# Performance work log

Measured on AMD Instinct MI355X. Metric: run time of the kernel, lower is better.

## Reference

```python
import jax, jax.numpy as jnp
import numpy as np


def _hard_sigmoid(x):
    # Keras ConvLSTM2D default recurrent_activation
    return jnp.clip(0.2 * x + 0.5, 0.0, 1.0)


def _conv(x, w):
    # NHWC input, HWIO kernel, SAME padding, stride 1
    return jax.lax.conv_general_dilated(
        x, w, (1, 1), 'SAME', dimension_numbers=('NHWC', 'HWIO', 'NHWC'))


def _convlstm(seq, h, c, k, rk, b):
    # seq: [B, T, H, W, Cin]; h, c: [B, H, W, F]
    # k: [kh, kw, Cin, 4F], rk: [kh, kw, F, 4F], b: [4F]
    def step(carry, x):
        h, c = carry
        z = _conv(x, k) + _conv(h, rk) + b  # [B,H,W,4F]
        zi, zf, zc, zo = jnp.split(z, 4, axis=-1)
        i = _hard_sigmoid(zi)
        f = _hard_sigmoid(zf)
        o = _hard_sigmoid(zo)
        c = f * c + i * jnp.tanh(zc)
        h = o * jnp.tanh(c)
        return (h, c), None
    (h, c), _ = jax.lax.scan(step, (h, c), jnp.swapaxes(seq, 0, 1))
    return h, c


def setup_inputs() -> dict:
    key = jax.random.key(0)
    ks = jax.random.split(key, 14)
    B, T, H, W, Cin, F, K = 32, 1, 64, 64, 1, 64, 3
    s = 0.05
    inp = {
        'input_': jax.random.normal(ks[0], (B, T, H, W, Cin), jnp.float32),
        'h0': jax.random.normal(ks[1], (B, H, W, F), jnp.float32) * s,
        'c0': jax.random.normal(ks[2], (B, H, W, F), jnp.float32) * s,
        'h1': jax.random.normal(ks[3], (B, H, W, F), jnp.float32) * s,
        'c1': jax.random.normal(ks[4], (B, H, W, F), jnp.float32) * s,
        'k0': jax.random.normal(ks[5], (K, K, Cin, 4 * F), jnp.float32) * s,
        'rk0': jax.random.normal(ks[6], (K, K, F, 4 * F), jnp.float32) * s,
        'b0': jnp.zeros((4 * F,), jnp.float32),
        'k1': jax.random.normal(ks[7], (K, K, F, 4 * F), jnp.float32) * s,
        'rk1': jax.random.normal(ks[8], (K, K, F, 4 * F), jnp.float32) * s,
        'b1': jnp.zeros((4 * F,), jnp.float32),
        'cw': jax.random.normal(ks[9], (1, 1, F, 1), jnp.float32) * s,
        'cb': jnp.zeros((1,), jnp.float32),
    }
    return inp


def reference(input_, h0, c0, h1, c1, k0, rk0, b0, k1, rk1, b1, cw, cb):
    # Layer 0 consumes the input frame sequence (T=1)
    h0n, c0n = _convlstm(input_, h0, c0, k0, rk0, b0)
    # Layer 1 consumes layer-0's last hidden state as its (length-1) input
    h1n, c1n = _convlstm(h0n[:, None], h1, c1, k1, rk1, b1)
    frames = _conv(h1n, cw) + cb  # 1x1 conv head -> [B,H,W,1]
    return frames, h0n, c0n, h1n, c1n
```

## Files before the change

### kernel.cpp

```cpp
#include <hip/hip_runtime.h>
#include <hip/hip_bf16.h>

typedef short s16;
typedef __attribute__((ext_vector_type(8))) short bf16x8;
typedef __attribute__((ext_vector_type(4))) float f32x4;

__device__ __forceinline__ s16 f2bf(float f) {
  unsigned u = __builtin_bit_cast(unsigned, f);
  unsigned r = (u + 0x7FFFu + ((u >> 16) & 1u)) >> 16;
  return (s16)r;
}

__device__ __forceinline__ float hsig(float x) {
  return fminf(fmaxf(0.2f * x + 0.5f, 0.0f), 1.0f);
}

__global__ void wprep_kernel(const float* __restrict__ rk0, const float* __restrict__ k1,
                             const float* __restrict__ rk1, const float* __restrict__ k0,
                             s16* __restrict__ w0q, s16* __restrict__ w1q,
                             s16* __restrict__ w2q, s16* __restrict__ k0t) {
  int idx = blockIdx.x * 256 + threadIdx.x;
  const int n1 = 18 * 8192;
  if (idx < 3 * n1) {
    int which = idx / n1;
    int i = idx - which * n1;
    int e    = i & 7;
    int lane = (i >> 3) & 63;
    int g    = (i >> 9) & 3;
    int j    = (i >> 11) & 3;
    int k    = (i >> 13) & 1;
    int tap  = i >> 14;
    int l15 = lane & 15, l4 = lane >> 4;
    int ic = k * 32 + l4 * 8 + e;
    int oc = j * 64 + g * 16 + l15;
    const float* src = (which == 0) ? rk0 : (which == 1) ? k1 : rk1;
    s16* dst = (which == 0) ? w0q : (which == 1) ? w1q : w2q;
    dst[i] = f2bf(src[(tap * 64 + ic) * 256 + oc]);
  } else if (idx < 3 * n1 + 8192) {
    int r = idx - 3 * n1;
    int kk = r & 31;
    int oc = r >> 5;
    k0t[r] = (kk < 9) ? f2bf(k0[kk * 256 + oc]) : (s16)0;
  }
}

#define PXS 66
#define ROWSZ (PXS * 64)
#define ASZ (6 * ROWSZ)

template <bool F32>
__device__ __forceinline__ bf16x8 load_conv8(const void* src, long off) {
  if constexpr (F32) {
    const float* p = (const float*)src + off;
    float4 v0 = *reinterpret_cast<const float4*>(p);
    float4 v1 = *reinterpret_cast<const float4*>(p + 4);
    bf16x8 r;
    r[0] = f2bf(v0.x); r[1] = f2bf(v0.y); r[2] = f2bf(v0.z); r[3] = f2bf(v0.w);
    r[4] = f2bf(v1.x); r[5] = f2bf(v1.y); r[6] = f2bf(v1.z); r[7] = f2bf(v1.w);
    return r;
  } else {
    return *reinterpret_cast<const bf16x8*>((const s16*)src + off);
  }
}

template <bool F32>
__device__ __forceinline__ void stage_src(s16* a_lds, const void* src, int b, int y0, int tid) {
  #pragma unroll
  for (int i = 0; i < 3; ++i) {
    int c   = tid + i * 1024;
    int row = c >> 9;
    int px  = (c >> 3) & 63;
    int cb  = c & 7;
    int y   = y0 - 1 + row;
    int xp  = px + 1;
    bf16x8 v = {};
    if ((unsigned)y < 64u)
      v = load_conv8<F32>(src, ((long)(b * 64 + y) * 64 + px) * 64 + cb * 8);
    *reinterpret_cast<bf16x8*>(a_lds + (row * PXS + xp) * 64 + ((cb ^ (xp & 7)) * 8)) = v;
  }
  if (tid < 96) {
    int row = tid >> 4;
    int xp  = ((tid >> 3) & 1) ? 65 : 0;
    int cb  = tid & 7;
    bf16x8 z = {};
    *reinterpret_cast<bf16x8*>(a_lds + (row * PXS + xp) * 64 + cb * 8) = z;
  }
}

template <int NSRC, bool XPATH, bool S0F32, bool S1F32>
__global__ __launch_bounds__(1024, 4) void cell_kernel(
    const void* __restrict__ src0,
    const void* __restrict__ src1,
    const s16* __restrict__ w0,
    const s16* __restrict__ w1,
    const float* __restrict__ xin,
    const s16* __restrict__ k0t,
    const float* __restrict__ bias,
    const float* __restrict__ c_old,
    float* __restrict__ h_out,
    float* __restrict__ c_out,
    s16* __restrict__ hb_out)
{
  __shared__ __align__(16) s16 a_lds[NSRC * ASZ];
  __shared__ __align__(16) s16 w_lds[2][8192];
  __shared__ float x_lds[XPATH ? 384 : 1];

  const int tid = threadIdx.x;
  const int b  = blockIdx.x >> 4;
  const int y0 = (blockIdx.x & 15) << 2;

  const int wave = tid >> 6;
  const int lane = tid & 63;
  const int g    = wave & 3;
  const int mh   = wave >> 2;
  const int l15  = lane & 15;
  const int l4   = lane >> 4;

  constexpr int NST = NSRC * 18;

  auto issueW = [&](int u) {
    int v = (u >= NST) ? u - NST : u;
    int si = (NSRC == 2 && v >= 18) ? 1 : 0;
    int vv = v - 18 * si;
    const s16* wt = (si ? w1 : w0) + vv * 8192;
    char* base = (char*)(&w_lds[0][0]) + (v & 1) * 16384 + (tid >> 6) * 1024;
    __builtin_amdgcn_global_load_lds(
        (const __attribute__((address_space(1))) void*)(wt + tid * 8),
        (__attribute__((address_space(3))) void*)base, 16, 0, 0);
  };

  auto readWf = [&](bf16x8 (&wf)[4], int slot) {
    const s16* wb = &w_lds[slot][0] + g * 512 + lane * 8;
    #pragma unroll
    for (int j = 0; j < 4; ++j)
      wf[j] = *reinterpret_cast<const bf16x8*>(wb + j * 2048);
  };

  f32x4 acc[4][4] = {};

  auto doStage = [&](const bf16x8 (&wf)[4], int u) {
    int si = (NSRC == 2 && u >= 18) ? 1 : 0;
    int uu = u - 18 * si;
    int tap = uu >> 1, kk = uu & 1;
    int dy = tap / 3, dx = tap - dy * 3;
    const char* sb = (const char*)a_lds + si * (ASZ * 2) + (mh + dy) * (ROWSZ * 2);
    bf16x8 af[4];
    #pragma unroll
    for (int m = 0; m < 4; ++m) {
      int xq   = m * 16 + l15 + dx;
      int boff = xq * 128 + ((((kk << 2) | l4) ^ (xq & 7)) << 4);
      af[m] = *reinterpret_cast<const bf16x8*>(sb + boff);
    }
    __builtin_amdgcn_s_setprio(1);
    #pragma unroll
    for (int m = 0; m < 4; ++m) {
      #pragma unroll
      for (int j = 0; j < 4; ++j)
        acc[m][j] = __builtin_amdgcn_mfma_f32_16x16x32_bf16(af[m], wf[j], acc[m][j], 0, 0, 0);
    }
    __builtin_amdgcn_s_setprio(0);
  };

  issueW(0);
  issueW(1);
  stage_src<S0F32>(a_lds, src0, b, y0, tid);
  if (NSRC == 2) stage_src<S1F32>(a_lds + ASZ, src1, b, y0, tid);
  if (XPATH) {
    if (tid < 384) {
      int row = tid >> 6, px = tid & 63;
      int y = y0 - 1 + row;
      x_lds[tid] = ((unsigned)y < 64u) ? xin[(b * 64 + y) * 64 + px] : 0.0f;
    }
  }
  __syncthreads();

  if (XPATH) {
    bf16x8 bx[4];
    #pragma unroll
    for (int j = 0; j < 4; ++j) {
      int oc = j * 64 + g * 16 + l15;
      bx[j] = *reinterpret_cast<const bf16x8*>(k0t + oc * 32 + l4 * 8);
    }
    #pragma unroll
    for (int m = 0; m < 4; ++m) {
      int px = m * 16 + l15;
      bf16x8 ax = {};
      #pragma unroll
      for (int e = 0; e < 8; ++e) {
        int t = l4 * 8 + e;
        if (t < 9) {
          int dyt = t / 3, dxt = t - dyt * 3;
          int xx = px + dxt - 1;
          float xv = ((unsigned)xx < 64u) ? x_lds[(mh + dyt) * 64 + xx] : 0.0f;
          ax[e] = f2bf(xv);
        }
      }
      #pragma unroll
      for (int j = 0; j < 4; ++j)
        acc[m][j] = __builtin_amdgcn_mfma_f32_16x16x32_bf16(ax, bx[j], acc[m][j], 0, 0, 0);
    }
  }

  bf16x8 wfA[4], wfB[4];
  readWf(wfA, 0);
  #pragma unroll
  for (int u = 0; u < NST; u += 2) {
    __builtin_amdgcn_s_barrier();
    issueW(u + 2);
    asm volatile("s_waitcnt vmcnt(1)" ::: "memory");
    __builtin_amdgcn_s_barrier();
    readWf(wfB, (u + 1) & 1);
    doStage(wfA, u);
    __builtin_amdgcn_s_barrier();
    issueW(u + 3);
    asm volatile("s_waitcnt vmcnt(1)" ::: "memory");
    __builtin_amdgcn_s_barrier();
    readWf(wfA, u & 1);
    doStage(wfB, u + 1);
  }

  float bi[4];
  #pragma unroll
  for (int j = 0; j < 4; ++j) bi[j] = bias[j * 64 + g * 16 + l15];

  const int pix_base = b * 4096 + y0 * 64;
  const int f = g * 16 + l15;
  #pragma unroll
  for (int m = 0; m < 4; ++m) {
    #pragma unroll
    for (int r = 0; r < 4; ++r) {
      int pl = mh * 64 + m * 16 + l4 * 4 + r;
      int off = (pix_base + pl) * 64 + f;
      float zi = acc[m][0][r] + bi[0];
      float zf = acc[m][1][r] + bi[1];
      float zc = acc[m][2][r] + bi[2];
      float zo = acc[m][3][r] + bi[3];
      float ig = hsig(zi), fg = hsig(zf), og = hsig(zo);
      float cn = fg * c_old[off] + ig * tanhf(zc);
      float hn = og * tanhf(cn);
      c_out[off] = cn;
      h_out[off] = hn;
      if (hb_out) hb_out[off] = f2bf(hn);
    }
  }
}

__global__ void frames_kernel(const float* __restrict__ h, const float* __restrict__ cw,
                              const float* __restrict__ cbp, float* __restrict__ out) {
  int tid = blockIdx.x * 256 + threadIdx.x;
  int p  = tid >> 2;
  int fc = (tid & 3) * 16;
  const float4* hp = reinterpret_cast<const float4*>(h + p * 64 + fc);
  const float4* wp = reinterpret_cast<const float4*>(cw + fc);
  float s = 0.0f;
  #pragma unroll
  for (int i = 0; i < 4; ++i) {
    float4 v = hp[i];
    float4 w = wp[i];
    s += v.x * w.x + v.y * w.y + v.z * w.z + v.w * w.w;
  }
  s += __shfl_xor(s, 1);
  s += __shfl_xor(s, 2);
  if ((tid & 3) == 0) out[p] = s + cbp[0];
}

extern "C" void kernel_launch(void* const* d_in, const int* in_sizes, int n_in,
                              void* d_out, int out_size, void* d_ws, size_t ws_size,
                              hipStream_t stream) {
  const float* x   = (const float*)d_in[0];
  const float* h0  = (const float*)d_in[1];
  const float* c0  = (const float*)d_in[2];
  const float* h1  = (const float*)d_in[3];
  const float* c1  = (const float*)d_in[4];
  const float* k0  = (const float*)d_in[5];
  const float* rk0 = (const float*)d_in[6];
  const float* b0  = (const float*)d_in[7];
  const float* k1  = (const float*)d_in[8];
  const float* rk1 = (const float*)d_in[9];
  const float* b1  = (const float*)d_in[10];
  const float* cw  = (const float*)d_in[11];
  const float* cbp = (const float*)d_in[12];

  float* out    = (float*)d_out;
  float* frames = out;
  float* h0n    = out + 131072;
  float* c0n    = out + 131072 + 8388608;
  float* h1n    = out + 131072 + 2 * 8388608;
  float* c1n    = out + 131072 + 3 * 8388608;

  char* ws = (char*)d_ws;
  const size_t SZ_H = 16777216;
  s16* h0nb = (s16*)(ws + 0 * SZ_H);
  s16* w0q  = (s16*)(ws + 1 * SZ_H);
  s16* w1q  = (s16*)(ws + 1 * SZ_H + 1 * 294912);
  s16* w2q  = (s16*)(ws + 1 * SZ_H + 2 * 294912);
  s16* k0t  = (s16*)(ws + 1 * SZ_H + 3 * 294912);

  wprep_kernel<<<1760, 256, 0, stream>>>(rk0, k1, rk1, k0, w0q, w1q, w2q, k0t);

  cell_kernel<1, true, true, false><<<512, 1024, 0, stream>>>(
      h0, nullptr, w0q, nullptr, x, k0t, b0, c0, h0n, c0n, h0nb);

  cell_kernel<2, false, false, true><<<512, 1024, 0, stream>>>(
      h0nb, h1, w1q, w2q, nullptr, nullptr, b1, c1, h1n, c1n, nullptr);

  frames_kernel<<<2048, 256, 0, stream>>>(h1n, cw, cbp, frames);
}
```

Baseline: 203.2 us.

## Use triple-buffered weight LDS ring with one barrier per stage

Moves the weight staging from a double buffer with register ping-pong to a three-slot LDS ring. This cuts each stage to a single wait plus barrier: the next load is issued, the current slot is read and the MFMAs run. It also relaxes launch bounds from 4 to 1 blocks per CU. The aim is to halve barrier count and simplify the schedule. The costs are more LDS per block and the loss of register-level prefetch of the next weight fragment, so LDS read latency is exposed before each stage.

```diff
diff --git a/kernel.cpp b/kernel.cpp
--- a/kernel.cpp
+++ b/kernel.cpp
@@ -14,6 +14,10 @@
 __device__ __forceinline__ float hsig(float x) {
   return fminf(fmaxf(0.2f * x + 0.5f, 0.0f), 1.0f);
 }
+
+#define PXS 66
+#define ROWSZ (PXS * 64)
+#define ASZ6 (6 * ROWSZ)
 
 __global__ void wprep_kernel(const float* __restrict__ rk0, const float* __restrict__ k1,
                              const float* __restrict__ rk1, const float* __restrict__ k0,
@@ -44,10 +48,6 @@
   }
 }
 
-#define PXS 66
-#define ROWSZ (PXS * 64)
-#define ASZ (6 * ROWSZ)
-
 template <bool F32>
 __device__ __forceinline__ bf16x8 load_conv8(const void* src, long off) {
   if constexpr (F32) {
@@ -64,7 +64,7 @@
 }
 
 template <bool F32>
-__device__ __forceinline__ void stage_src(s16* a_lds, const void* src, int b, int y0, int tid) {
+__device__ __forceinline__ void stage6(s16* a_lds, const void* src, int b, int y0, int tid) {
   #pragma unroll
   for (int i = 0; i < 3; ++i) {
     int c   = tid + i * 1024;
@@ -88,7 +88,7 @@
 }
 
 template <int NSRC, bool XPATH, bool S0F32, bool S1F32>
-__global__ __launch_bounds__(1024, 4) void cell_kernel(
+__global__ __launch_bounds__(1024, 1) void cell_kernel(
     const void* __restrict__ src0,
     const void* __restrict__ src1,
     const s16* __restrict__ w0,
@@ -101,8 +101,8 @@
     float* __restrict__ c_out,
     s16* __restrict__ hb_out)
 {
-  __shared__ __align__(16) s16 a_lds[NSRC * ASZ];
-  __shared__ __align__(16) s16 w_lds[2][8192];
+  __shared__ __align__(16) s16 a_lds[NSRC * ASZ6];
+  __shared__ __align__(16) s16 w_lds[3][8192];
   __shared__ float x_lds[XPATH ? 384 : 1];
 
   const int tid = threadIdx.x;
@@ -123,7 +123,7 @@
     int si = (NSRC == 2 && v >= 18) ? 1 : 0;
     int vv = v - 18 * si;
     const s16* wt = (si ? w1 : w0) + vv * 8192;
-    char* base = (char*)(&w_lds[0][0]) + (v & 1) * 16384 + (tid >> 6) * 1024;
+    char* base = (char*)(&w_lds[0][0]) + (v % 3) * 16384 + (tid >> 6) * 1024;
     __builtin_amdgcn_global_load_lds(
         (const __attribute__((address_space(1))) void*)(wt + tid * 8),
         (__attribute__((address_space(3))) void*)base, 16, 0, 0);
@@ -143,7 +143,7 @@
     int uu = u - 18 * si;
     int tap = uu >> 1, kk = uu & 1;
     int dy = tap / 3, dx = tap - dy * 3;
-    const char* sb = (const char*)a_lds + si * (ASZ * 2) + (mh + dy) * (ROWSZ * 2);
+    const char* sb = (const char*)a_lds + si * (ASZ6 * 2) + (mh + dy) * (ROWSZ * 2);
     bf16x8 af[4];
     #pragma unroll
     for (int m = 0; m < 4; ++m) {
@@ -163,8 +163,8 @@
 
   issueW(0);
   issueW(1);
-  stage_src<S0F32>(a_lds, src0, b, y0, tid);
-  if (NSRC == 2) stage_src<S1F32>(a_lds + ASZ, src1, b, y0, tid);
+  stage6<S0F32>(a_lds, src0, b, y0, tid);
+  if (NSRC == 2) stage6<S1F32>(a_lds + ASZ6, src1, b, y0, tid);
   if (XPATH) {
     if (tid < 384) {
       int row = tid >> 6, px = tid & 63;
@@ -201,22 +201,15 @@
     }
   }
 
-  bf16x8 wfA[4], wfB[4];
-  readWf(wfA, 0);
-  #pragma unroll
-  for (int u = 0; u < NST; u += 2) {
-    __builtin_amdgcn_s_barrier();
-    issueW(u + 2);
+  bf16x8 wf[4];
+  #pragma unroll
+  for (int u = 0; u < NST; ++u) {
     asm volatile("s_waitcnt vmcnt(1)" ::: "memory");
     __builtin_amdgcn_s_barrier();
-    readWf(wfB, (u + 1) & 1);
-    doStage(wfA, u);
-    __builtin_amdgcn_s_barrier();
-    issueW(u + 3);
-    asm volatile("s_waitcnt vmcnt(1)" ::: "memory");
-    __builtin_amdgcn_s_barrier();
-    readWf(wfA, u & 1);
-    doStage(wfB, u + 1);
+    __builtin_amdgcn_sched_barrier(0);
+    issueW(u + 2);
+    readWf(wf, u % 3);
+    doStage(wf, u);
   }
 
   float bi[4];
```

New measurement: 185.5 us. 8.7% less time.

## Halve row tile per block, quad-buffer weights, and prefetch A fragments

Applied to the files above, without the earlier changes.

Each block now covers 2 image rows instead of 4, which doubles the grid to 1024 blocks and halves per-wave M tiles (2x16 pixels). Weight staging moves from a double to a quad LDS ring, so each step needs one barrier instead of two, and A fragments are now read one stage ahead alongside the weights. This aims for better CU fill and less barrier stalling. In exchange, each weight tile is reused across half as many pixels, so global weight traffic per output doubles and halo rows are loaded twice as often.

```diff
diff --git a/kernel.cpp b/kernel.cpp
--- a/kernel.cpp
+++ b/kernel.cpp
@@ -14,6 +14,10 @@
 __device__ __forceinline__ float hsig(float x) {
   return fminf(fmaxf(0.2f * x + 0.5f, 0.0f), 1.0f);
 }
+
+#define PXS 66
+#define ROWSZ (PXS * 64)
+#define ASZ4 (4 * ROWSZ)
 
 __global__ void wprep_kernel(const float* __restrict__ rk0, const float* __restrict__ k1,
                              const float* __restrict__ rk1, const float* __restrict__ k0,
@@ -44,10 +48,6 @@
   }
 }
 
-#define PXS 66
-#define ROWSZ (PXS * 64)
-#define ASZ (6 * ROWSZ)
-
 template <bool F32>
 __device__ __forceinline__ bf16x8 load_conv8(const void* src, long off) {
   if constexpr (F32) {
@@ -64,9 +64,9 @@
 }
 
 template <bool F32>
-__device__ __forceinline__ void stage_src(s16* a_lds, const void* src, int b, int y0, int tid) {
-  #pragma unroll
-  for (int i = 0; i < 3; ++i) {
+__device__ __forceinline__ void stage4(s16* a_lds, const void* src, int b, int y0, int tid) {
+  #pragma unroll
+  for (int i = 0; i < 2; ++i) {
     int c   = tid + i * 1024;
     int row = c >> 9;
     int px  = (c >> 3) & 63;
@@ -78,7 +78,7 @@
       v = load_conv8<F32>(src, ((long)(b * 64 + y) * 64 + px) * 64 + cb * 8);
     *reinterpret_cast<bf16x8*>(a_lds + (row * PXS + xp) * 64 + ((cb ^ (xp & 7)) * 8)) = v;
   }
-  if (tid < 96) {
+  if (tid < 64) {
     int row = tid >> 4;
     int xp  = ((tid >> 3) & 1) ? 65 : 0;
     int cb  = tid & 7;
@@ -101,18 +101,18 @@
     float* __restrict__ c_out,
     s16* __restrict__ hb_out)
 {
-  __shared__ __align__(16) s16 a_lds[NSRC * ASZ];
-  __shared__ __align__(16) s16 w_lds[2][8192];
-  __shared__ float x_lds[XPATH ? 384 : 1];
+  __shared__ __align__(16) s16 a_lds[NSRC * ASZ4];
+  __shared__ __align__(16) s16 w_lds[4][8192];
+  __shared__ float x_lds[XPATH ? 256 : 1];
 
   const int tid = threadIdx.x;
-  const int b  = blockIdx.x >> 4;
-  const int y0 = (blockIdx.x & 15) << 2;
+  const int b  = blockIdx.x >> 5;
+  const int y0 = (blockIdx.x & 31) << 1;
 
   const int wave = tid >> 6;
   const int lane = tid & 63;
   const int g    = wave & 3;
-  const int mh   = wave >> 2;
+  const int mq   = wave >> 2;
   const int l15  = lane & 15;
   const int l4   = lane >> 4;
 
@@ -123,37 +123,40 @@
     int si = (NSRC == 2 && v >= 18) ? 1 : 0;
     int vv = v - 18 * si;
     const s16* wt = (si ? w1 : w0) + vv * 8192;
-    char* base = (char*)(&w_lds[0][0]) + (v & 1) * 16384 + (tid >> 6) * 1024;
+    char* base = (char*)(&w_lds[0][0]) + (u & 3) * 16384 + (tid >> 6) * 1024;
     __builtin_amdgcn_global_load_lds(
         (const __attribute__((address_space(1))) void*)(wt + tid * 8),
         (__attribute__((address_space(3))) void*)base, 16, 0, 0);
   };
 
-  auto readWf = [&](bf16x8 (&wf)[4], int slot) {
-    const s16* wb = &w_lds[slot][0] + g * 512 + lane * 8;
+  auto readWf = [&](bf16x8 (&wf)[4], int u) {
+    const s16* wb = &w_lds[u & 3][0] + g * 512 + lane * 8;
     #pragma unroll
     for (int j = 0; j < 4; ++j)
       wf[j] = *reinterpret_cast<const bf16x8*>(wb + j * 2048);
   };
 
-  f32x4 acc[4][4] = {};
-
-  auto doStage = [&](const bf16x8 (&wf)[4], int u) {
-    int si = (NSRC == 2 && u >= 18) ? 1 : 0;
-    int uu = u - 18 * si;
+  auto readA = [&](bf16x8 (&af)[2], int u) {
+    int v = (u >= NST) ? u - NST : u;
+    int si = (NSRC == 2 && v >= 18) ? 1 : 0;
+    int uu = v - 18 * si;
     int tap = uu >> 1, kk = uu & 1;
     int dy = tap / 3, dx = tap - dy * 3;
-    const char* sb = (const char*)a_lds + si * (ASZ * 2) + (mh + dy) * (ROWSZ * 2);
-    bf16x8 af[4];
-    #pragma unroll
-    for (int m = 0; m < 4; ++m) {
-      int xq   = m * 16 + l15 + dx;
+    const char* sb = (const char*)a_lds + si * (ASZ4 * 2) + ((mq >> 1) + dy) * (ROWSZ * 2);
+    #pragma unroll
+    for (int m = 0; m < 2; ++m) {
+      int xq   = (mq & 1) * 32 + m * 16 + l15 + dx;
       int boff = xq * 128 + ((((kk << 2) | l4) ^ (xq & 7)) << 4);
       af[m] = *reinterpret_cast<const bf16x8*>(sb + boff);
     }
+  };
+
+  f32x4 acc[2][4] = {};
+
+  auto doMfma = [&](const bf16x8 (&af)[2], const bf16x8 (&wf)[4]) {
     __builtin_amdgcn_s_setprio(1);
     #pragma unroll
-    for (int m = 0; m < 4; ++m) {
+    for (int m = 0; m < 2; ++m) {
       #pragma unroll
       for (int j = 0; j < 4; ++j)
         acc[m][j] = __builtin_amdgcn_mfma_f32_16x16x32_bf16(af[m], wf[j], acc[m][j], 0, 0, 0);
@@ -163,10 +166,11 @@
 
   issueW(0);
   issueW(1);
-  stage_src<S0F32>(a_lds, src0, b, y0, tid);
-  if (NSRC == 2) stage_src<S1F32>(a_lds + ASZ, src1, b, y0, tid);
+  issueW(2);
+  stage4<S0F32>(a_lds, src0, b, y0, tid);
+  if (NSRC == 2) stage4<S1F32>(a_lds + ASZ4, src1, b, y0, tid);
   if (XPATH) {
-    if (tid < 384) {
+    if (tid < 256) {
       int row = tid >> 6, px = tid & 63;
       int y = y0 - 1 + row;
       x_lds[tid] = ((unsigned)y < 64u) ? xin[(b * 64 + y) * 64 + px] : 0.0f;
@@ -175,15 +179,10 @@
   __syncthreads();
 
   if (XPATH) {
-    bf16x8 bx[4];
-    #pragma unroll
-    for (int j = 0; j < 4; ++j) {
-      int oc = j * 64 + g * 16 + l15;
-      bx[j] = *reinterpret_cast<const bf16x8*>(k0t + oc * 32 + l4 * 8);
-    }
-    #pragma unroll
-    for (int m = 0; m < 4; ++m) {
-      int px = m * 16 + l15;
+    const int rb = mq >> 1;
+    #pragma unroll
+    for (int m = 0; m < 2; ++m) {
+      int px = (mq & 1) * 32 + m * 16 + l15;
       bf16x8 ax = {};
       #pragma unroll
       for (int e = 0; e < 8; ++e) {
@@ -191,32 +190,36 @@
         if (t < 9) {
           int dyt = t / 3, dxt = t - dyt * 3;
           int xx = px + dxt - 1;
-          float xv = ((unsigned)xx < 64u) ? x_lds[(mh + dyt) * 64 + xx] : 0.0f;
+          float xv = ((unsigned)xx < 64u) ? x_lds[(rb + dyt) * 64 + xx] : 0.0f;
           ax[e] = f2bf(xv);
         }
       }
       #pragma unroll
-      for (int j = 0; j < 4; ++j)
-        acc[m][j] = __builtin_amdgcn_mfma_f32_16x16x32_bf16(ax, bx[j], acc[m][j], 0, 0, 0);
-    }
-  }
-
-  bf16x8 wfA[4], wfB[4];
+      for (int j = 0; j < 4; ++j) {
+        int oc = j * 64 + g * 16 + l15;
+        bf16x8 bx = *reinterpret_cast<const bf16x8*>(k0t + oc * 32 + l4 * 8);
+        acc[m][j] = __builtin_amdgcn_mfma_f32_16x16x32_bf16(ax, bx, acc[m][j], 0, 0, 0);
+      }
+    }
+  }
+
+  bf16x8 afA[2], afB[2], wfA[4], wfB[4];
+  readA(afA, 0);
   readWf(wfA, 0);
   #pragma unroll
   for (int u = 0; u < NST; u += 2) {
-    __builtin_amdgcn_s_barrier();
-    issueW(u + 2);
     asm volatile("s_waitcnt vmcnt(1)" ::: "memory");
     __builtin_amdgcn_s_barrier();
-    readWf(wfB, (u + 1) & 1);
-    doStage(wfA, u);
-    __builtin_amdgcn_s_barrier();
     issueW(u + 3);
+    readA(afB, u + 1);
+    readWf(wfB, u + 1);
+    doMfma(afA, wfA);
     asm volatile("s_waitcnt vmcnt(1)" ::: "memory");
     __builtin_amdgcn_s_barrier();
-    readWf(wfA, u & 1);
-    doStage(wfB, u + 1);
+    issueW(u + 4);
+    readA(afA, u + 2);
+    readWf(wfA, u + 2);
+    doMfma(afB, wfB);
   }
 
   float bi[4];
@@ -226,10 +229,10 @@
   const int pix_base = b * 4096 + y0 * 64;
   const int f = g * 16 + l15;
   #pragma unroll
-  for (int m = 0; m < 4; ++m) {
+  for (int m = 0; m < 2; ++m) {
     #pragma unroll
     for (int r = 0; r < 4; ++r) {
-      int pl = mh * 64 + m * 16 + l4 * 4 + r;
+      int pl = mq * 32 + m * 16 + l4 * 4 + r;
       int off = (pix_base + pl) * 64 + f;
       float zi = acc[m][0][r] + bi[0];
       float zf = acc[m][1][r] + bi[1];
@@ -298,10 +301,10 @@
 
   wprep_kernel<<<1760, 256, 0, stream>>>(rk0, k1, rk1, k0, w0q, w1q, w2q, k0t);
 
-  cell_kernel<1, true, true, false><<<512, 1024, 0, stream>>>(
+  cell_kernel<1, true, true, false><<<1024, 1024, 0, stream>>>(
       h0, nullptr, w0q, nullptr, x, k0t, b0, c0, h0n, c0n, h0nb);
 
-  cell_kernel<2, false, false, true><<<512, 1024, 0, stream>>>(
+  cell_kernel<2, false, false, true><<<1024, 1024, 0, stream>>>(
       h0nb, h1, w1q, w2q, nullptr, nullptr, b1, c1, h1n, c1n, nullptr);
 
   frames_kernel<<<2048, 256, 0, stream>>>(h1n, cw, cbp, frames);
```

New measurement: 188.8 us. 7.1% less time.
